# Kernel tuning notes

Hardware: AMD Instinct MI355X
Metric: run time of the kernel (lower is better)

Reference implementation:

```python
import jax, jax.numpy as jnp
import numpy as np

DIM = 32      # feature dim (must be small: unnormalized det prod overflows fp32 otherwise)
K = 16        # number of mixture components / experts
B = 262144    # batch


def setup_inputs() -> dict:
    key = jax.random.key(0)
    k0, k1, k2, k3, k4 = jax.random.split(key, 5)
    x = jax.random.normal(k0, (B, DIM), dtype=jnp.float32)
    xavier = 1.0 / np.sqrt(DIM / 2.0)
    mu = (jax.random.normal(k1, (K, DIM), dtype=jnp.float32) * xavier)
    # torch init is ones; use small values so prod(2*pi*sigma2) stays finite in fp32
    logsigma = jax.random.normal(k2, (K, DIM), dtype=jnp.float32) * 0.1
    W = jax.random.normal(k3, (K, DIM, DIM), dtype=jnp.float32) * (1.0 / np.sqrt(DIM))
    b = jax.random.normal(k4, (K, DIM), dtype=jnp.float32) * 0.01
    return {"x": x, "mu": mu, "logsigma": logsigma, "W": W, "b": b}


def reference(x, mu, logsigma, W, b):
    # Gaussian prior pdf per expert, vectorized over k
    two_pi = np.float32(2.0 * np.pi)
    sigma2 = jnp.exp(2.0 * logsigma)                                   # [k, d]
    const = jax.lax.rsqrt(jnp.prod(two_pi * sigma2, axis=-1))           # [k]
    diff = x[None, :, :] - mu[:, None, :]                               # [k, b, d]
    exponent = -0.5 * jnp.sum(diff * diff / sigma2[:, None, :], axis=-1)  # [k, b]
    ps = const[:, None] * jnp.exp(exponent)                             # [k, b]
    w = ps / jnp.sum(ps, axis=0, keepdims=True)                         # [k, b]
    # per-expert Linear (torch convention: x @ W_k.T + b_k) + ReLU
    lik = jax.nn.relu(jnp.einsum('bd,kod->kbo', x, W) + b[:, None, :])  # [k, b, d]
    # gate-weighted sum over experts
    return jnp.einsum('kb,kbo->bo', w, lik)                             # [b, d]
```

## Files before the change

### kernel.cpp

```cpp
#include <hip/hip_runtime.h>
#include <math.h>

#define DIM 32
#define NK  16
#define LOG2E 1.4426950408889634f

typedef __attribute__((ext_vector_type(8))) short bf16x8;
typedef __attribute__((ext_vector_type(4))) float f32x4;

#define MFMA16 __builtin_amdgcn_mfma_f32_16x16x32_bf16

#define WHI_OFF 0
#define WLO_OFF 32768
#define HH_OFF  65536
#define HL_OFF  66560
#define GH_OFF  67584
#define GL_OFF  68608
#define CG_OFF  69632

typedef __attribute__((address_space(1))) const unsigned int gu32;
typedef __attribute__((address_space(3))) unsigned int lu32;

__device__ __forceinline__ void split2(float x, short* hi, short* lo) {
  unsigned u = __float_as_uint(x);
  *hi = (short)(u >> 16);
  float hf = __uint_as_float(u & 0xFFFF0000u);
  float l = x - hf;
  *lo = (short)(__float_as_uint(l) >> 16);
}

__global__ __launch_bounds__(256) void gmm_setup_kernel(
    const float* __restrict__ mu, const float* __restrict__ logsigma,
    const float* __restrict__ W, char* __restrict__ ws)
{
  int i = blockIdx.x * 256 + threadIdx.x;
  short* whi = (short*)(ws + WHI_OFF);
  short* wlo = (short*)(ws + WLO_OFF);
  if (i < NK * DIM * DIM) split2(W[i], &whi[i], &wlo[i]);
  if (i < NK * DIM) {
    float s2 = __expf(2.0f * logsigma[i]);
    float h = (-0.5f / s2) * LOG2E;
    float g = (mu[i] / s2) * LOG2E;
    short a, b;
    split2(h, &a, &b);
    ((short*)(ws + HH_OFF))[i] = a; ((short*)(ws + HL_OFF))[i] = b;
    split2(g, &a, &b);
    ((short*)(ws + GH_OFF))[i] = a; ((short*)(ws + GL_OFF))[i] = b;
  }
  if (i < NK) {
    float acc = 0.0f;
    for (int d = 0; d < DIM; ++d) {
      float s2 = __expf(2.0f * logsigma[i * DIM + d]);
      float m  = mu[i * DIM + d];
      acc += m * m * (-0.5f / s2) * LOG2E - 0.5f * log2f(6.283185307179586f * s2);
    }
    ((float*)(ws + CG_OFF))[i] = acc;
  }
}

__global__ __launch_bounds__(512, 4) void gmm_moe_kernel(
    const float* __restrict__ x,
    const float* __restrict__ bias,
    const char* __restrict__ ws,
    float* __restrict__ out)
{
  __shared__ char lds_w[65536];
  const int tid  = threadIdx.x;
  const int wid  = tid >> 6;
  const int lane = tid & 63;
  const int g = lane >> 4;
  const int c = lane & 15;
  const int sbase = (blockIdx.x * 8 + wid) * 32;

  #pragma unroll
  for (int r = 0; r < 8; ++r) {
    const int off = r * 8192 + wid * 1024;
    __builtin_amdgcn_global_load_lds(
        (gu32*)(ws + off + lane * 16), (lu32*)(lds_w + off), 16, 0, 0);
  }

  float4 xa[2][2];
  #pragma unroll
  for (int t = 0; t < 2; ++t) {
    const float4* xp =
        (const float4*)(x + (size_t)(sbase + t * 16 + c) * DIM + g * 8);
    xa[t][0] = xp[0];
    xa[t][1] = xp[1];
  }

  const bf16x8 fhh = ((const bf16x8*)(ws + HH_OFF))[c * 4 + g];
  const bf16x8 fhl = ((const bf16x8*)(ws + HL_OFF))[c * 4 + g];
  const bf16x8 fgh = ((const bf16x8*)(ws + GH_OFF))[c * 4 + g];
  const bf16x8 fgl = ((const bf16x8*)(ws + GL_OFF))[c * 4 + g];
  const float  cgv = ((const float*)(ws + CG_OFF))[c];

  bf16x8 xh[2], xl[2];
  f32x4 wv[2];
  #pragma unroll
  for (int t = 0; t < 2; ++t) {
    float xv[8] = {xa[t][0].x, xa[t][0].y, xa[t][0].z, xa[t][0].w,
                   xa[t][1].x, xa[t][1].y, xa[t][1].z, xa[t][1].w};
    bf16x8 x2h, x2l;
    #pragma unroll
    for (int j = 0; j < 8; ++j) {
      short h_, l_;
      split2(xv[j], &h_, &l_);
      xh[t][j] = h_; xl[t][j] = l_;
      float q = xv[j] * xv[j];
      split2(q, &h_, &l_);
      x2h[j] = h_; x2l[j] = l_;
    }
    f32x4 e = {cgv, cgv, cgv, cgv};
    e = MFMA16(x2h,   fhh, e, 0, 0, 0);
    e = MFMA16(x2l,   fhh, e, 0, 0, 0);
    e = MFMA16(x2h,   fhl, e, 0, 0, 0);
    e = MFMA16(xh[t], fgh, e, 0, 0, 0);
    e = MFMA16(xl[t], fgh, e, 0, 0, 0);
    e = MFMA16(xh[t], fgl, e, 0, 0, 0);
    #pragma unroll
    for (int r = 0; r < 4; ++r) {
      float p = __builtin_amdgcn_exp2f(e[r]);
      float s = p;
      s += __shfl_xor(s, 1, 64);
      s += __shfl_xor(s, 2, 64);
      s += __shfl_xor(s, 4, 64);
      s += __shfl_xor(s, 8, 64);
      wv[t][r] = p * __builtin_amdgcn_rcpf(s);
    }
  }

  __syncthreads();

  f32x4 o0[2], o1[2];
  #pragma unroll
  for (int t = 0; t < 2; ++t) { o0[t] = (f32x4){0,0,0,0}; o1[t] = (f32x4){0,0,0,0}; }

  const int wbase = c * 64 + g * 16;
  #pragma unroll
  for (int k = 0; k < NK; ++k) {
    const bf16x8 w0h = *(const bf16x8*)(lds_w + k * 2048 + wbase);
    const bf16x8 w1h = *(const bf16x8*)(lds_w + k * 2048 + 1024 + wbase);
    const bf16x8 w0l = *(const bf16x8*)(lds_w + 32768 + k * 2048 + wbase);
    const bf16x8 w1l = *(const bf16x8*)(lds_w + 32768 + k * 2048 + 1024 + wbase);
    const float b0 = bias[k * DIM + c];
    const float b1 = bias[k * DIM + 16 + c];
    #pragma unroll
    for (int t = 0; t < 2; ++t) {
      f32x4 s0 = {b0, b0, b0, b0}, s1 = {b1, b1, b1, b1};
      s0 = MFMA16(xh[t], w0h, s0, 0, 0, 0);
      s0 = MFMA16(xl[t], w0h, s0, 0, 0, 0);
      s0 = MFMA16(xh[t], w0l, s0, 0, 0, 0);
      s1 = MFMA16(xh[t], w1h, s1, 0, 0, 0);
      s1 = MFMA16(xl[t], w1h, s1, 0, 0, 0);
      s1 = MFMA16(xh[t], w1l, s1, 0, 0, 0);
      f32x4 wb;
      #pragma unroll
      for (int r = 0; r < 4; ++r)
        wb[r] = __shfl(wv[t][r], (lane & 48) | k, 64);
      const f32x4 z = {0.0f, 0.0f, 0.0f, 0.0f};
      o0[t] = __builtin_elementwise_fma(wb, __builtin_elementwise_max(s0, z), o0[t]);
      o1[t] = __builtin_elementwise_fma(wb, __builtin_elementwise_max(s1, z), o1[t]);
    }
  }

  #pragma unroll
  for (int t = 0; t < 2; ++t) {
    #pragma unroll
    for (int r = 0; r < 4; ++r) {
      size_t row = (size_t)(sbase + t * 16 + g * 4 + r);
      out[row * DIM + c]      = o0[t][r];
      out[row * DIM + 16 + c] = o1[t][r];
    }
  }
}

extern "C" void kernel_launch(void* const* d_in, const int* in_sizes, int n_in,
                              void* d_out, int out_size, void* d_ws, size_t ws_size,
                              hipStream_t stream) {
  const float* x  = (const float*)d_in[0];
  const float* mu = (const float*)d_in[1];
  const float* ls = (const float*)d_in[2];
  const float* W  = (const float*)d_in[3];
  const float* bv = (const float*)d_in[4];
  float* out = (float*)d_out;
  const int B = in_sizes[0] / DIM;

  gmm_setup_kernel<<<(NK * DIM * DIM + 255) / 256, 256, 0, stream>>>(
      mu, ls, W, (char*)d_ws);
  gmm_moe_kernel<<<B / 256, 512, 0, stream>>>(x, bv, (const char*)d_ws, out);
}
```

Baseline: 117.4 us.

## Pre-swizzle W into MFMA fragments, stage only hi half in LDS, gates via LDS

The setup kernel now writes W hi/lo in MFMA fragment order, so each lane reads a contiguous 16-byte fragment. Only the hi half of W is staged in LDS; the lo half is read directly from global memory, where it should stay cached. Per-sample gate weights are written to a padded LDS buffer and read back as vectors, replacing four cross-lane shuffles per expert per tile. Blocks shrink to 4 waves with smaller LDS, trading occupancy and more global-load latency in the inner loop for less LDS pressure and fewer shuffles.

```diff
diff --git a/kernel.cpp b/kernel.cpp
--- a/kernel.cpp
+++ b/kernel.cpp
@@ -10,8 +10,8 @@
 
 #define MFMA16 __builtin_amdgcn_mfma_f32_16x16x32_bf16
 
-#define WHI_OFF 0
-#define WLO_OFF 32768
+#define WHIF_OFF 0
+#define WLOF_OFF 32768
 #define HH_OFF  65536
 #define HL_OFF  66560
 #define GH_OFF  67584
@@ -20,6 +20,10 @@
 
 typedef __attribute__((address_space(1))) const unsigned int gu32;
 typedef __attribute__((address_space(3))) unsigned int lu32;
+
+#define LDSP_BASE 32768
+#define LDSP_WAVE 2304
+#define LDS_TOTAL (32768 + 4 * LDSP_WAVE)
 
 __device__ __forceinline__ void split2(float x, short* hi, short* lo) {
   unsigned u = __float_as_uint(x);
@@ -34,9 +38,20 @@
     const float* __restrict__ W, char* __restrict__ ws)
 {
   int i = blockIdx.x * 256 + threadIdx.x;
-  short* whi = (short*)(ws + WHI_OFF);
-  short* wlo = (short*)(ws + WLO_OFF);
-  if (i < NK * DIM * DIM) split2(W[i], &whi[i], &wlo[i]);
+  if (i < NK * 2 * 64) {
+    const int k = i >> 7, o16 = (i >> 6) & 1, lane = i & 63;
+    const int c = lane & 15, g = lane >> 4;
+    const int o = o16 * 16 + c;
+    bf16x8 hi, lo;
+    #pragma unroll
+    for (int j = 0; j < 8; ++j) {
+      short h_, l_;
+      split2(W[(k * DIM + o) * DIM + g * 8 + j], &h_, &l_);
+      hi[j] = h_; lo[j] = l_;
+    }
+    ((bf16x8*)(ws + WHIF_OFF))[i] = hi;
+    ((bf16x8*)(ws + WLOF_OFF))[i] = lo;
+  }
   if (i < NK * DIM) {
     float s2 = __expf(2.0f * logsigma[i]);
     float h = (-0.5f / s2) * LOG2E;
@@ -58,25 +73,25 @@
   }
 }
 
-__global__ __launch_bounds__(512, 4) void gmm_moe_kernel(
+__global__ __launch_bounds__(256, 3) void gmm_moe_kernel(
     const float* __restrict__ x,
     const float* __restrict__ bias,
     const char* __restrict__ ws,
     float* __restrict__ out)
 {
-  __shared__ char lds_w[65536];
+  __shared__ char lds[LDS_TOTAL];
   const int tid  = threadIdx.x;
   const int wid  = tid >> 6;
   const int lane = tid & 63;
   const int g = lane >> 4;
   const int c = lane & 15;
-  const int sbase = (blockIdx.x * 8 + wid) * 32;
+  const int sbase = (blockIdx.x * 4 + wid) * 32;
 
   #pragma unroll
   for (int r = 0; r < 8; ++r) {
-    const int off = r * 8192 + wid * 1024;
+    const int off = r * 4096 + wid * 1024;
     __builtin_amdgcn_global_load_lds(
-        (gu32*)(ws + off + lane * 16), (lu32*)(lds_w + off), 16, 0, 0);
+        (gu32*)(ws + WHIF_OFF + off + lane * 16), (lu32*)(lds + off), 16, 0, 0);
   }
 
   float4 xa[2][2];
@@ -129,19 +144,26 @@
     }
   }
 
+  {
+    char* pw = lds + LDSP_BASE + wid * LDSP_WAVE + c * 144 + g * 16;
+    *(f32x4*)(pw)      = wv[0];
+    *(f32x4*)(pw + 64) = wv[1];
+  }
+
   __syncthreads();
 
+  const bf16x8* wlof = (const bf16x8*)(ws + WLOF_OFF);
+  const char*   ldsp = lds + LDSP_BASE + wid * LDSP_WAVE + g * 16;
   f32x4 o0[2], o1[2];
   #pragma unroll
   for (int t = 0; t < 2; ++t) { o0[t] = (f32x4){0,0,0,0}; o1[t] = (f32x4){0,0,0,0}; }
 
-  const int wbase = c * 64 + g * 16;
   #pragma unroll
   for (int k = 0; k < NK; ++k) {
-    const bf16x8 w0h = *(const bf16x8*)(lds_w + k * 2048 + wbase);
-    const bf16x8 w1h = *(const bf16x8*)(lds_w + k * 2048 + 1024 + wbase);
-    const bf16x8 w0l = *(const bf16x8*)(lds_w + 32768 + k * 2048 + wbase);
-    const bf16x8 w1l = *(const bf16x8*)(lds_w + 32768 + k * 2048 + 1024 + wbase);
+    const bf16x8 w0h = *(const bf16x8*)(lds + (k * 2 + 0) * 1024 + lane * 16);
+    const bf16x8 w1h = *(const bf16x8*)(lds + (k * 2 + 1) * 1024 + lane * 16);
+    const bf16x8 w0l = wlof[(k * 2 + 0) * 64 + lane];
+    const bf16x8 w1l = wlof[(k * 2 + 1) * 64 + lane];
     const float b0 = bias[k * DIM + c];
     const float b1 = bias[k * DIM + 16 + c];
     #pragma unroll
@@ -153,10 +175,7 @@
       s1 = MFMA16(xh[t], w1h, s1, 0, 0, 0);
       s1 = MFMA16(xl[t], w1h, s1, 0, 0, 0);
       s1 = MFMA16(xh[t], w1l, s1, 0, 0, 0);
-      f32x4 wb;
-      #pragma unroll
-      for (int r = 0; r < 4; ++r)
-        wb[r] = __shfl(wv[t][r], (lane & 48) | k, 64);
+      const f32x4 wb = *(const f32x4*)(ldsp + k * 144 + t * 64);
       const f32x4 z = {0.0f, 0.0f, 0.0f, 0.0f};
       o0[t] = __builtin_elementwise_fma(wb, __builtin_elementwise_max(s0, z), o0[t]);
       o1[t] = __builtin_elementwise_fma(wb, __builtin_elementwise_max(s1, z), o1[t]);
@@ -185,7 +204,6 @@
   float* out = (float*)d_out;
   const int B = in_sizes[0] / DIM;
 
-  gmm_setup_kernel<<<(NK * DIM * DIM + 255) / 256, 256, 0, stream>>>(
-      mu, ls, W, (char*)d_ws);
-  gmm_moe_kernel<<<B / 256, 512, 0, stream>>>(x, bv, (const char*)d_ws, out);
-}
+  gmm_setup_kernel<<<8, 256, 0, stream>>>(mu, ls, W, (char*)d_ws);
+  gmm_moe_kernel<<<B / 128, 256, 0, stream>>>(x, bv, (const char*)d_ws, out);
+}
```

Result: no change. 116.0 us (-1.2%).
